# Kernel tuning notes

Hardware: AMD Instinct MI355X
Metric: run time of the kernel (lower is better)

The kernel has to match this reference:

```python
import jax, jax.numpy as jnp
import numpy as np


def conv1x1(x, w, b):
    # x: (B,C,H,W), w: (O,C), b: (O,)
    return jnp.einsum('bchw,oc->bohw', x, w) + b[None, :, None, None]


def maxpool2x2(x):
    B, C, H, W = x.shape
    return x.reshape(B, C, H // 2, 2, W // 2, 2).max(axis=(3, 5))


def setup_inputs() -> dict:
    key = jax.random.key(0)
    ks = jax.random.split(key, 10)
    B, C, H, W = 16, 256, 64, 64
    K = 8
    ck, ch = C // K, C // 2  # 32, 128
    sc = lambda fan_in: 1.0 / np.sqrt(fan_in)
    return {
        'x': jax.random.normal(ks[0], (B, C, H, W), jnp.float32),
        'wf': jax.random.normal(ks[1], (ck, C), jnp.float32) * sc(C),
        'bf': jnp.zeros((ck,), jnp.float32),
        'wg': jax.random.normal(ks[2], (ck, C), jnp.float32) * sc(C),
        'bg': jnp.zeros((ck,), jnp.float32),
        'wh': jax.random.normal(ks[3], (ch, C), jnp.float32) * sc(C),
        'bh': jnp.zeros((ch,), jnp.float32),
        'wv': jax.random.normal(ks[4], (C, ch), jnp.float32) * sc(ch),
        'bv': jnp.zeros((C,), jnp.float32),
        'gamma': jnp.float32(0.5),  # nonzero so the attention branch matters
    }


def reference(x, wf, bf, wg, bg, wh, bh, wv, bv, gamma):
    B, C, H, W = x.shape
    HW = H * W
    f = conv1x1(x, wf, bf).reshape(B, -1, HW)            # (B, C/K, HW)
    g = maxpool2x2(conv1x1(x, wg, bg))                    # (B, C/K, H/2, W/2)
    h = maxpool2x2(conv1x1(x, wh, bh))                    # (B, C/2, H/2, W/2)
    HWp = HW // 4
    g = g.reshape(B, -1, HWp)
    h = h.reshape(B, -1, HWp)
    s = jnp.einsum('bck,bcl->bkl', f, g)                  # (B, HW, HW')
    beta = jax.nn.softmax(s, axis=-1)
    o = jnp.einsum('bjk,blk->bjl', h, beta)               # (B, C/2, HW)
    o = o.reshape(B, -1, H, W)
    return gamma * conv1x1(o, wv, bv) + x
```

## Files before the change

### kernel.cpp

```cpp
#include <hip/hip_runtime.h>
#include <hip/hip_bf16.h>
#include <stdint.h>

#define B_N   16
#define C_N   256
#define W_N   64
#define HW_N  4096
#define CK_N  32
#define CH_N  128
#define HWP_N 1024
#define MR_N  192

typedef __attribute__((ext_vector_type(8))) short short8;
typedef __attribute__((ext_vector_type(4))) short short4v;
typedef __attribute__((ext_vector_type(4))) float f32x4;

#define MFMA(a, b, c) __builtin_amdgcn_mfma_f32_16x16x32_bf16((a), (b), (c), 0, 0, 0)

__device__ __forceinline__ f32x4 MFMA16B(short4v a, short4v b, f32x4 c) {
#if __has_builtin(__builtin_amdgcn_mfma_f32_16x16x16bf16_1k)
    return __builtin_amdgcn_mfma_f32_16x16x16bf16_1k(a, b, c, 0, 0, 0);
#else
    asm("v_mfma_f32_16x16x16_bf16 %0, %1, %2, %0" : "+v"(c) : "v"(a), "v"(b));
    return c;
#endif
}

__device__ __forceinline__ unsigned short f2bf(float f) {
    union { float f; unsigned u; } v; v.f = f;
    unsigned r = v.u + 0x7FFFu + ((v.u >> 16) & 1u);
    return (unsigned short)(r >> 16);
}
__device__ __forceinline__ unsigned packrn(float lo, float hi) {
    unsigned a = __float_as_uint(lo) + 0x8000u;
    unsigned b = __float_as_uint(hi) + 0x8000u;
    return __builtin_amdgcn_perm(b, a, 0x07060302);
}
__device__ __forceinline__ short8 ld8(const void* p) {
    return *reinterpret_cast<const short8*>(p);
}

__global__ __launch_bounds__(256) void k_prep(
    const float* __restrict__ wf, const float* __restrict__ wg,
    const float* __restrict__ wh, const float* __restrict__ wv,
    unsigned short* __restrict__ Wc, unsigned short* __restrict__ Wv)
{
    int i = blockIdx.x * 256 + threadIdx.x;
    if (i < MR_N * C_N) {
        int r = i / C_N, c = i % C_N;
        float v = (r < 32) ? wf[r * C_N + c]
                : (r < 64) ? wg[(r - 32) * C_N + c]
                           : wh[(r - 64) * C_N + c];
        Wc[i] = f2bf(v);
    }
    if (i < C_N * CH_N) Wv[i] = f2bf(wv[i]);
}

__global__ __launch_bounds__(256) void k_conv_fgh(
    const float* __restrict__ x, const unsigned short* __restrict__ Wc,
    const float* __restrict__ bfp, const float* __restrict__ bgp, const float* __restrict__ bhp,
    unsigned short* __restrict__ f_, unsigned short* __restrict__ g_, unsigned short* __restrict__ h_)
{
    __shared__ __align__(16) unsigned char lds[64 * 512];
    const int T = threadIdx.x;
    const int lane = T & 63, wid = T >> 6;
    const int blk = blockIdx.x;
    const int b = blk >> 6;
    const int seg = blk & 63;
    const int rp = seg >> 1;
    const int half = seg & 1;
    const float* xb = x + (size_t)b * C_N * HW_N;

    #pragma unroll
    for (int i = 0; i < 8; ++i) {
        int task = i * 256 + T;
        int pq = task & 15;
        int cp = task >> 4;
        int px0 = pq * 4;
        int row = 2 * rp + (px0 >> 5);
        int wcol = half * 32 + (px0 & 31);
        const float4 v0 = *reinterpret_cast<const float4*>(xb + (size_t)(2 * cp) * HW_N + row * W_N + wcol);
        const float4 v1 = *reinterpret_cast<const float4*>(xb + (size_t)(2 * cp + 1) * HW_N + row * W_N + wcol);
        float vlo[4] = {v0.x, v0.y, v0.z, v0.w};
        float vhi[4] = {v1.x, v1.y, v1.z, v1.w};
        int kc = cp >> 2, co = cp & 3;
        #pragma unroll
        for (int j = 0; j < 4; ++j) {
            int px = px0 + j;
            *reinterpret_cast<unsigned*>(lds + px * 512 + ((kc ^ (px & 31)) << 4) + co * 4)
                = packrn(vlo[j], vhi[j]);
        }
    }
    __syncthreads();

    const int l15 = lane & 15, quad = lane >> 4;
    f32x4 acc[3][4];
    #pragma unroll
    for (int mt = 0; mt < 3; ++mt)
        #pragma unroll
        for (int nt = 0; nt < 4; ++nt)
            acc[mt][nt] = f32x4{0.f, 0.f, 0.f, 0.f};

    const int m0base = wid * 48;
    for (int k0 = 0; k0 < 256; k0 += 32) {
        short8 afr[3];
        #pragma unroll
        for (int mt = 0; mt < 3; ++mt)
            afr[mt] = ld8(Wc + (size_t)(m0base + mt * 16 + l15) * C_N + k0 + quad * 8);
        #pragma unroll
        for (int nt = 0; nt < 4; ++nt) {
            int px = nt * 16 + l15;
            int kc = (k0 >> 3) + quad;
            short8 bfr = ld8(lds + px * 512 + ((kc ^ (px & 31)) << 4));
            #pragma unroll
            for (int mt = 0; mt < 3; ++mt)
                acc[mt][nt] = MFMA(afr[mt], bfr, acc[mt][nt]);
        }
    }

    #pragma unroll
    for (int mt = 0; mt < 3; ++mt) {
        int mbase = m0base + mt * 16;
        int mrow0 = mbase + quad * 4;
        float bias[4];
        #pragma unroll
        for (int r = 0; r < 4; ++r) {
            int m = mrow0 + r;
            bias[r] = (m < 32) ? bfp[m] : (m < 64) ? bgp[m - 32] : bhp[m - 64];
        }
        if (mbase < 32) {
            #pragma unroll
            for (int nt = 0; nt < 4; ++nt) {
                int px = nt * 16 + l15;
                int p = (2 * rp + (px >> 5)) * W_N + half * 32 + (px & 31);
                uint2 u;
                u.x = packrn(acc[mt][nt][0] + bias[0], acc[mt][nt][1] + bias[1]);
                u.y = packrn(acc[mt][nt][2] + bias[2], acc[mt][nt][3] + bias[3]);
                *reinterpret_cast<uint2*>(f_ + ((size_t)b * HW_N + p) * CK_N + mrow0) = u;
            }
        } else if (mbase < 64) {
            int gc0 = mrow0 - 32;
            #pragma unroll
            for (int nt = 0; nt < 2; ++nt) {
                float pv[4];
                #pragma unroll
                for (int r = 0; r < 4; ++r) {
                    float m1 = fmaxf(acc[mt][nt][r], acc[mt][nt + 2][r]);
                    pv[r] = fmaxf(m1, __shfl_xor(m1, 1)) + bias[r];
                }
                if ((lane & 1) == 0) {
                    int kp = rp * 32 + half * 16 + ((nt * 16 + l15) >> 1);
                    uint2 u;
                    u.x = packrn(pv[0], pv[1]);
                    u.y = packrn(pv[2], pv[3]);
                    *reinterpret_cast<uint2*>(g_ + ((size_t)b * HWP_N + kp) * CK_N + gc0) = u;
                }
            }
        } else {
            int hc0 = mrow0 - 64;
            #pragma unroll
            for (int nt = 0; nt < 2; ++nt) {
                float pv[4];
                #pragma unroll
                for (int r = 0; r < 4; ++r) {
                    float m1 = fmaxf(acc[mt][nt][r], acc[mt][nt + 2][r]);
                    pv[r] = fmaxf(m1, __shfl_xor(m1, 1)) + bias[r];
                }
                #pragma unroll
                for (int r = 0; r < 4; ++r) {
                    int lo = (int)(packrn(pv[r], pv[r]) & 0xFFFFu);
                    int hi = __shfl_down(lo, 2);
                    if ((lane & 3) == 0) {
                        int kp2 = rp * 32 + half * 16 + nt * 8 + (l15 >> 1);
                        *reinterpret_cast<unsigned*>(
                            h_ + ((size_t)b * CH_N + hc0 + r) * HWP_N + kp2)
                            = (unsigned)lo | ((unsigned)hi << 16);
                    }
                }
            }
        }
    }
}

__global__ __launch_bounds__(256, 4) void k_attn(
    const unsigned short* __restrict__ f_, const unsigned short* __restrict__ g_,
    const unsigned short* __restrict__ h_, unsigned short* __restrict__ o_)
{
    __shared__ __align__(16) unsigned char Vl[2 * 17408];
    const int T = threadIdx.x;
    const int lane = T & 63, wid = T >> 6;
    const int l15 = lane & 15, quad = lane >> 4;

    const int blk = blockIdx.x;
    const int b = blk >> 6;
    const int q0w = (blk & 63) * 64 + wid * 16;
    const unsigned short* fb = f_ + (size_t)b * HW_N * CK_N;
    const unsigned short* gb = g_ + (size_t)b * HWP_N * CK_N;
    const unsigned short* hb = h_ + (size_t)b * CH_N * HWP_N;

    short8 ffr = ld8(fb + (size_t)(q0w + l15) * CK_N + quad * 8);

    const f32x4 zf = {0.f, 0.f, 0.f, 0.f};
    f32x4 oacc[8];
    #pragma unroll
    for (int ct = 0; ct < 8; ++ct)
        oacc[ct] = f32x4{0.f, 0.f, 0.f, 0.f};
    float lsum = 0.f;

    const int sch = T >> 3, skq = T & 7;
    uint4 vpre[4];
    #pragma unroll
    for (int i = 0; i < 4; ++i)
        vpre[i] = *reinterpret_cast<const uint4*>(hb + (size_t)(sch + i * 32) * HWP_N + skq * 8);
    short8 gcur[4];
    #pragma unroll
    for (int kt = 0; kt < 4; ++kt)
        gcur[kt] = ld8(gb + (size_t)(kt * 16 + l15) * CK_N + quad * 8);

    for (int c = 0; c < 16; ++c) {
        unsigned char* buf = Vl + (c & 1) * 17408;
        #pragma unroll
        for (int i = 0; i < 4; ++i) {
            unsigned char* dst = buf + (sch + i * 32) * 136 + skq * 16;
            *reinterpret_cast<uint2*>(dst)     = uint2{vpre[i].x, vpre[i].y};
            *reinterpret_cast<uint2*>(dst + 8) = uint2{vpre[i].z, vpre[i].w};
        }
        if (c < 15) {
            #pragma unroll
            for (int i = 0; i < 4; ++i)
                vpre[i] = *reinterpret_cast<const uint4*>(
                    hb + (size_t)(sch + i * 32) * HWP_N + (c + 1) * 64 + skq * 8);
        }
        __syncthreads();

        f32x4 sp[4];
        #pragma unroll
        for (int kt = 0; kt < 4; ++kt)
            sp[kt] = MFMA(gcur[kt], ffr, zf);
        if (c < 15) {
            #pragma unroll
            for (int kt = 0; kt < 4; ++kt)
                gcur[kt] = ld8(gb + (size_t)((c + 1) * 64 + kt * 16 + l15) * CK_N + quad * 8);
        }

        short4v pf[4];
        float lw = 0.f;
        #pragma unroll
        for (int kt = 0; kt < 4; ++kt) {
            float p0 = __builtin_amdgcn_exp2f(sp[kt][0] * 1.44269504f - 28.85390082f);
            float p1 = __builtin_amdgcn_exp2f(sp[kt][1] * 1.44269504f - 28.85390082f);
            float p2 = __builtin_amdgcn_exp2f(sp[kt][2] * 1.44269504f - 28.85390082f);
            float p3 = __builtin_amdgcn_exp2f(sp[kt][3] * 1.44269504f - 28.85390082f);
            lw += (p0 + p1) + (p2 + p3);
            uint2 u{packrn(p0, p1), packrn(p2, p3)};
            pf[kt] = __builtin_bit_cast(short4v, u);
        }
        lsum += lw;

        const int vbase = l15 * 136 + quad * 8;
        #pragma unroll
        for (int ct = 0; ct < 8; ++ct) {
            #pragma unroll
            for (int kt = 0; kt < 4; ++kt) {
                short4v afr = *reinterpret_cast<const short4v*>(buf + vbase + ct * 2176 + kt * 32);
                oacc[ct] = MFMA16B(afr, pf[kt], oacc[ct]);
            }
        }
    }

    lsum += __shfl_xor(lsum, 16); lsum += __shfl_xor(lsum, 32);
    const float rl = 1.f / lsum;
    unsigned short* ob = o_ + (size_t)b * HW_N * CH_N;
    const int q = q0w + l15;
    #pragma unroll
    for (int ct = 0; ct < 8; ++ct) {
        uint2 u;
        u.x = packrn(oacc[ct][0] * rl, oacc[ct][1] * rl);
        u.y = packrn(oacc[ct][2] * rl, oacc[ct][3] * rl);
        *reinterpret_cast<uint2*>(ob + (size_t)q * CH_N + ct * 16 + quad * 4) = u;
    }
}

__global__ __launch_bounds__(256, 4) void k_out(
    const unsigned short* __restrict__ o_, const unsigned short* __restrict__ Wv,
    const float* __restrict__ bv, const float* __restrict__ x,
    const float* __restrict__ gamma_p, float* __restrict__ out)
{
    const int T = threadIdx.x;
    const int lane = T & 63, wid = T >> 6;
    const int l15 = lane & 15, quad = lane >> 4;
    const int w = blockIdx.x * 4 + wid;
    const int b = w >> 8;
    const int rem = w & 255;
    const int oc0 = (rem >> 6) * 64;
    const int px0 = (rem & 63) * 64;
    const unsigned short* ob = o_ + ((size_t)b * HW_N + px0) * CH_N;

    f32x4 acc[4][4];
    #pragma unroll
    for (int mt = 0; mt < 4; ++mt)
        #pragma unroll
        for (int nt = 0; nt < 4; ++nt)
            acc[mt][nt] = f32x4{0.f, 0.f, 0.f, 0.f};

    #pragma unroll
    for (int k0 = 0; k0 < 128; k0 += 32) {
        short8 bfr[4];
        #pragma unroll
        for (int nt = 0; nt < 4; ++nt)
            bfr[nt] = ld8(ob + (size_t)(nt * 16 + l15) * CH_N + k0 + quad * 8);
        #pragma unroll
        for (int mt = 0; mt < 4; ++mt) {
            short8 afr = ld8(Wv + (size_t)(oc0 + mt * 16 + l15) * CH_N + k0 + quad * 8);
            #pragma unroll
            for (int nt = 0; nt < 4; ++nt)
                acc[mt][nt] = MFMA(bfr[nt], afr, acc[mt][nt]);
        }
    }

    const float gamma = *gamma_p;
    const float* xb = x + (size_t)b * C_N * HW_N;
    float* outb = out + (size_t)b * C_N * HW_N;
    #pragma unroll
    for (int mt = 0; mt < 4; ++mt) {
        int oc = oc0 + mt * 16 + l15;
        float bvv = bv[oc];
        #pragma unroll
        for (int nt = 0; nt < 4; ++nt) {
            size_t base = (size_t)oc * HW_N + px0 + nt * 16 + quad * 4;
            float4 xv = *reinterpret_cast<const float4*>(xb + base);
            float4 ov;
            ov.x = gamma * (acc[mt][nt][0] + bvv) + xv.x;
            ov.y = gamma * (acc[mt][nt][1] + bvv) + xv.y;
            ov.z = gamma * (acc[mt][nt][2] + bvv) + xv.z;
            ov.w = gamma * (acc[mt][nt][3] + bvv) + xv.w;
            *reinterpret_cast<float4*>(outb + base) = ov;
        }
    }
}

extern "C" void kernel_launch(void* const* d_in, const int* in_sizes, int n_in,
                              void* d_out, int out_size, void* d_ws, size_t ws_size,
                              hipStream_t stream) {
    const float* x     = (const float*)d_in[0];
    const float* wf    = (const float*)d_in[1];
    const float* bf    = (const float*)d_in[2];
    const float* wg    = (const float*)d_in[3];
    const float* bg    = (const float*)d_in[4];
    const float* wh    = (const float*)d_in[5];
    const float* bh    = (const float*)d_in[6];
    const float* wv    = (const float*)d_in[7];
    const float* bv    = (const float*)d_in[8];
    const float* gamma = (const float*)d_in[9];
    float* out = (float*)d_out;
    char* ws = (char*)d_ws;

    unsigned short* f_ = (unsigned short*)(ws);
    unsigned short* g_ = (unsigned short*)(ws + 4194304);
    unsigned short* h_ = (unsigned short*)(ws + 5242880);
    unsigned short* o_ = (unsigned short*)(ws + 9437184);
    unsigned short* Wc = (unsigned short*)(ws + 26214400);
    unsigned short* Wv = (unsigned short*)(ws + 26312704);

    k_prep<<<192, 256, 0, stream>>>(wf, wg, wh, wv, Wc, Wv);
    k_conv_fgh<<<1024, 256, 0, stream>>>(x, Wc, bf, bg, bh, f_, g_, h_);
    k_attn<<<1024, 256, 0, stream>>>(f_, g_, h_, o_);
    k_out<<<1024, 256, 0, stream>>>(o_, Wv, bv, x, gamma, out);
}
```

Baseline: 207.2 us.

## Use 16x16x32 bf16 MFMA for PV product with permuted key ordering

The attention kernel's P·V product now uses the K=32 bf16 MFMA instead of the K=16 variant, halving the number of MFMA issues and LDS reads per chunk. G rows are loaded in a permuted key order so the S-tile output registers line up with the K=32 B-operand layout. The V tile in LDS gets a 144-byte row stride so each lane does 16-byte reads and writes. This costs more shared memory per block and relies on the index permutation being exactly right.

```diff
diff --git a/kernel.cpp b/kernel.cpp
--- a/kernel.cpp
+++ b/kernel.cpp
@@ -12,19 +12,10 @@
 #define MR_N  192
 
 typedef __attribute__((ext_vector_type(8))) short short8;
-typedef __attribute__((ext_vector_type(4))) short short4v;
 typedef __attribute__((ext_vector_type(4))) float f32x4;
+typedef __attribute__((ext_vector_type(4))) unsigned uint4v;
 
 #define MFMA(a, b, c) __builtin_amdgcn_mfma_f32_16x16x32_bf16((a), (b), (c), 0, 0, 0)
-
-__device__ __forceinline__ f32x4 MFMA16B(short4v a, short4v b, f32x4 c) {
-#if __has_builtin(__builtin_amdgcn_mfma_f32_16x16x16bf16_1k)
-    return __builtin_amdgcn_mfma_f32_16x16x16bf16_1k(a, b, c, 0, 0, 0);
-#else
-    asm("v_mfma_f32_16x16x16_bf16 %0, %1, %2, %0" : "+v"(c) : "v"(a), "v"(b));
-    return c;
-#endif
-}
 
 __device__ __forceinline__ unsigned short f2bf(float f) {
     union { float f; unsigned u; } v; v.f = f;
@@ -186,7 +177,7 @@
     const unsigned short* __restrict__ f_, const unsigned short* __restrict__ g_,
     const unsigned short* __restrict__ h_, unsigned short* __restrict__ o_)
 {
-    __shared__ __align__(16) unsigned char Vl[2 * 17408];
+    __shared__ __align__(16) unsigned char Vl[2 * 18432];
     const int T = threadIdx.x;
     const int lane = T & 63, wid = T >> 6;
     const int l15 = lane & 15, quad = lane >> 4;
@@ -208,6 +199,8 @@
     float lsum = 0.f;
 
     const int sch = T >> 3, skq = T & 7;
+    const int kq = ((l15 >> 2) << 3) | (l15 & 3);
+
     uint4 vpre[4];
     #pragma unroll
     for (int i = 0; i < 4; ++i)
@@ -215,16 +208,13 @@
     short8 gcur[4];
     #pragma unroll
     for (int kt = 0; kt < 4; ++kt)
-        gcur[kt] = ld8(gb + (size_t)(kt * 16 + l15) * CK_N + quad * 8);
+        gcur[kt] = ld8(gb + (size_t)(((kt >> 1) << 5) + ((kt & 1) << 2) + kq) * CK_N + quad * 8);
 
     for (int c = 0; c < 16; ++c) {
-        unsigned char* buf = Vl + (c & 1) * 17408;
-        #pragma unroll
-        for (int i = 0; i < 4; ++i) {
-            unsigned char* dst = buf + (sch + i * 32) * 136 + skq * 16;
-            *reinterpret_cast<uint2*>(dst)     = uint2{vpre[i].x, vpre[i].y};
-            *reinterpret_cast<uint2*>(dst + 8) = uint2{vpre[i].z, vpre[i].w};
-        }
+        unsigned char* buf = Vl + (c & 1) * 18432;
+        #pragma unroll
+        for (int i = 0; i < 4; ++i)
+            *reinterpret_cast<uint4*>(buf + (sch + i * 32) * 144 + skq * 16) = vpre[i];
         if (c < 15) {
             #pragma unroll
             for (int i = 0; i < 4; ++i)
@@ -240,10 +230,10 @@
         if (c < 15) {
             #pragma unroll
             for (int kt = 0; kt < 4; ++kt)
-                gcur[kt] = ld8(gb + (size_t)((c + 1) * 64 + kt * 16 + l15) * CK_N + quad * 8);
-        }
-
-        short4v pf[4];
+                gcur[kt] = ld8(gb + (size_t)((c + 1) * 64 + ((kt >> 1) << 5) + ((kt & 1) << 2) + kq) * CK_N + quad * 8);
+        }
+
+        unsigned pw[8];
         float lw = 0.f;
         #pragma unroll
         for (int kt = 0; kt < 4; ++kt) {
@@ -252,19 +242,20 @@
             float p2 = __builtin_amdgcn_exp2f(sp[kt][2] * 1.44269504f - 28.85390082f);
             float p3 = __builtin_amdgcn_exp2f(sp[kt][3] * 1.44269504f - 28.85390082f);
             lw += (p0 + p1) + (p2 + p3);
-            uint2 u{packrn(p0, p1), packrn(p2, p3)};
-            pf[kt] = __builtin_bit_cast(short4v, u);
+            pw[2 * kt]     = packrn(p0, p1);
+            pw[2 * kt + 1] = packrn(p2, p3);
         }
         lsum += lw;
-
-        const int vbase = l15 * 136 + quad * 8;
+        short8 pfA = __builtin_bit_cast(short8, uint4v{pw[0], pw[1], pw[2], pw[3]});
+        short8 pfB = __builtin_bit_cast(short8, uint4v{pw[4], pw[5], pw[6], pw[7]});
+
+        const int vbase = l15 * 144 + quad * 16;
         #pragma unroll
         for (int ct = 0; ct < 8; ++ct) {
-            #pragma unroll
-            for (int kt = 0; kt < 4; ++kt) {
-                short4v afr = *reinterpret_cast<const short4v*>(buf + vbase + ct * 2176 + kt * 32);
-                oacc[ct] = MFMA16B(afr, pf[kt], oacc[ct]);
-            }
+            short8 a0 = *reinterpret_cast<const short8*>(buf + vbase + ct * 2304);
+            oacc[ct] = MFMA(a0, pfA, oacc[ct]);
+            short8 a1 = *reinterpret_cast<const short8*>(buf + vbase + ct * 2304 + 64);
+            oacc[ct] = MFMA(a1, pfB, oacc[ct]);
         }
     }
 
```

New measurement: 255.9 us. 23.5% more time.
